# Kernel optimization log

Measured on AMD Instinct MI355X. Metric: run time of the kernel, lower is better.

## Reference

```python
import jax, jax.numpy as jnp
import numpy as np

EPS = 1.1920929e-07  # torch float32 eps used by nn.RMSNorm(elementwise_affine=False)
MAX_LR = 0.01        # default_step_transform_max_lr


def rmsnorm(x):
    return x * jax.lax.rsqrt(jnp.mean(jnp.square(x), axis=-1, keepdims=True) + EPS)


def assoc_scan(gates, inputs):
    # first-order recurrence x_t = gates_t * x_{t-1} + inputs_t along axis=1
    gates = jnp.broadcast_to(gates, inputs.shape)

    def combine(a, b):
        ag, ax = a
        bg, bx = b
        return (ag * bg, bg * ax + bx)

    _, out = jax.lax.associative_scan(combine, (gates, inputs), axis=1)
    return out


def setup_inputs():
    key = jax.random.key(0)
    ks = jax.random.split(key, 12)
    b, t, dim, heads, d, c = 4, 8192, 512, 8, 64, 64
    di = heads * d
    sc_dim = dim ** -0.5
    sc_d = d ** -0.5
    return {
        'seq': jax.random.normal(ks[0], (b, t, dim), jnp.float32),
        'w1': jax.random.normal(ks[1], (d, d), jnp.float32) * sc_d,
        'w2': jax.random.normal(ks[2], (d, d), jnp.float32) * sc_d,
        'Wq': jax.random.normal(ks[3], (dim, di), jnp.float32) * sc_dim,
        'Wkv': jax.random.normal(ks[4], (dim, 2 * di), jnp.float32) * sc_dim,
        'Wstep': jax.random.normal(ks[5], (dim, heads), jnp.float32) * sc_dim,
        'Wmom': jax.random.normal(ks[6], (dim, heads), jnp.float32) * sc_dim,
        'Wdecay': jax.random.normal(ks[7], (dim, heads), jnp.float32) * sc_dim,
        'Wgate': jax.random.normal(ks[8], (dim, heads), jnp.float32) * sc_dim,
        'Wcombine': jax.random.normal(ks[9], (di, dim), jnp.float32) * (di ** -0.5),
        'gamma': jnp.zeros((heads, 1, d), jnp.float32),
        'chunk_size': 64,
    }


def _forward(seq, w1, w2, Wq, Wkv, Wstep, Wmom, Wdecay, Wgate, Wcombine, gamma, c):
    b, t, dim = seq.shape
    heads = Wstep.shape[1]
    d = w1.shape[0]
    n = t // c          # number of chunks (seq_len assumed multiple of chunk_size)
    bh = b * heads

    # ---------------- store_memories ----------------
    s = rmsnorm(seq)  # store_norm
    # adaptive per-token lr: sigmoid * max_lr, per head -> (bh, n, c)
    lr = jax.nn.sigmoid(jnp.einsum('btd,dh->bth', s, Wstep)) * MAX_LR
    lr = lr.transpose(0, 2, 1).reshape(bh, n, c)
    # per-chunk momentum / decay gates from chunk-mean of seq
    s_chunk = s.reshape(b, n, c, dim).mean(axis=2)
    mom_gate = jax.nn.sigmoid(jnp.einsum('bnd,dh->bnh', s_chunk, Wmom)).transpose(0, 2, 1).reshape(bh, n, 1)
    decay = jax.nn.sigmoid(jnp.einsum('bnd,dh->bnh', s_chunk, Wdecay)).transpose(0, 2, 1).reshape(bh, n, 1)
    # keys / values, split heads, chunked -> (bh, n, c, d)
    kv = jnp.einsum('btd,de->bte', s, Wkv)
    k, v = jnp.split(kv, 2, axis=-1)
    split = lambda x: x.reshape(b, t, heads, d).transpose(0, 2, 1, 3).reshape(bh, n, c, d)
    k, v = split(k), split(v)

    def chunk_loss(ws, kc, lrc, vc):
        x = kc @ ws[0]
        x = jax.nn.silu(x) @ ws[1]
        return jnp.sum(jnp.mean(jnp.square(x - vc), axis=-1) * lrc)

    # per-sample (per bh, per chunk) grads of the tiny MLP
    grad_fn = jax.grad(chunk_loss, argnums=0)
    g1, g2 = jax.vmap(jax.vmap(grad_fn, in_axes=(None, 0, 0, 0)), in_axes=(None, 0, 0, 0))((w1, w2), k, lr, v)

    updates = []
    for g in (g1, g2):
        flat = (-g).reshape(bh, n, d * d)        # surprises
        momentum = assoc_scan(mom_gate, flat)     # momentum recurrence
        upd = assoc_scan(1.0 - decay, momentum)   # decayed weight-update recurrence
        updates.append(upd.reshape(bh, n, d, d))

    # ---------------- retrieve_memories ----------------
    r = rmsnorm(seq)[:, c - 1:]                   # retrieve_norm + causal shift
    pad = (-r.shape[1]) % c                       # pad to multiple of chunk_size (= c-1 here)
    r = jnp.pad(r, ((0, 0), (0, pad), (0, 0)))    # (b, n*c, dim)
    q = jnp.einsum('btd,de->bte', r, Wq)
    qs = q.reshape(b, n * c, heads, d).transpose(0, 2, 1, 3).reshape(bh, n, c, d)
    # apply per-chunk fast weights (base + update)
    x = jnp.einsum('bncd,bnde->bnce', qs, w1 + updates[0])
    x = jax.nn.silu(x)
    x = jnp.einsum('bncd,bnde->bnce', x, w2 + updates[1])
    vals = x.reshape(b, heads, n * c, d)
    vals = rmsnorm(vals) * (gamma + 1.0)          # MultiheadRMSNorm (gamma zeros-init)
    gate = jax.nn.sigmoid(jnp.einsum('btd,dh->bth', r, Wgate))  # retrieve_gate
    vals = vals * gate.transpose(0, 2, 1)[..., None]
    out = vals.transpose(0, 2, 1, 3).reshape(b, n * c, heads * d)  # merge heads
    out = jnp.einsum('bte,ed->btd', out, Wcombine)                 # combine_heads
    out = jnp.pad(out, ((0, 0), (c - 1, 0), (0, 0)))[:, :t]       # shift back, crop
    return out


def reference(seq, w1, w2, Wq, Wkv, Wstep, Wmom, Wdecay, Wgate, Wcombine, gamma, chunk_size):
    return _forward(seq, w1, w2, Wq, Wkv, Wstep, Wmom, Wdecay, Wgate, Wcombine, gamma, chunk_size)
```

## Files before the change

### kernel.cpp

```cpp
#include <hip/hip_runtime.h>
#include <cstdint>

#define EPS     1.1920929e-07f
#define MAX_LR  0.01f
#define BB      4
#define TT      8192
#define DIMM    512
#define HH      8
#define DD      64
#define CC      64
#define NN      128
#define BHH     32
#define LDSP    72

typedef __attribute__((ext_vector_type(8))) short short8;
typedef __attribute__((ext_vector_type(4))) float f32x4;

__device__ __forceinline__ float sigmoidf_(float x){ return 1.0f/(1.0f+__expf(-x)); }
__device__ __forceinline__ float bf2f(uint32_t lo16){ return __uint_as_float(lo16<<16); }
__device__ __forceinline__ uint16_t f2bf(float f){
    uint32_t x = __float_as_uint(f);
    return (uint16_t)((x + 0x7fffu + ((x>>16)&1u)) >> 16);
}
__device__ __forceinline__ uint32_t pk2(float a, float b){
    return (uint32_t)f2bf(a) | ((uint32_t)f2bf(b)<<16);
}
__device__ __forceinline__ void gload_lds16(const uint16_t* g, uint16_t* l){
    __builtin_amdgcn_global_load_lds(
        (const __attribute__((address_space(1))) unsigned int*)g,
        (__attribute__((address_space(3))) unsigned int*)l, 16, 0, 0);
}

__device__ __forceinline__ void gemm64(const uint16_t* A, const uint16_t* B,
                                       int strip, int q, int col, f32x4* acc)
{
    #pragma unroll
    for (int ks=0; ks<64; ks+=32){
        short8 af = *(const short8*)&A[(strip*16+col)*LDSP + ks + q*8];
        #pragma unroll
        for (int nt=0;nt<4;nt++){
            short8 bf = *(const short8*)&B[(nt*16+col)*LDSP + ks + q*8];
            acc[nt] = __builtin_amdgcn_mfma_f32_16x16x32_bf16(af, bf, acc[nt], 0,0,0);
        }
    }
}

__device__ __forceinline__ void gemm64g(const uint16_t* __restrict__ Ag,
                                        const uint16_t* B,
                                        int strip, int q, int col, f32x4* acc)
{
    #pragma unroll
    for (int ks=0; ks<64; ks+=32){
        short8 af = *(const short8*)&Ag[(strip*16+col)*DD + ks + q*8];
        #pragma unroll
        for (int nt=0;nt<4;nt++){
            short8 bf = *(const short8*)&B[(nt*16+col)*LDSP + ks + q*8];
            acc[nt] = __builtin_amdgcn_mfma_f32_16x16x32_bf16(af, bf, acc[nt], 0,0,0);
        }
    }
}

__global__ __launch_bounds__(256) void k_scale(
    const float* __restrict__ seq, float* __restrict__ scale,
    uint16_t* __restrict__ sbf)
{
    int wave = threadIdx.x >> 6, lane = threadIdx.x & 63;
    int row = blockIdx.x*4 + wave;
    const float4* sp = (const float4*)&seq[(size_t)row*DIMM + lane*8];
    float4 x0 = sp[0], x1 = sp[1];
    float ss = x0.x*x0.x + x0.y*x0.y + x0.z*x0.z + x0.w*x0.w
             + x1.x*x1.x + x1.y*x1.y + x1.z*x1.z + x1.w*x1.w;
    #pragma unroll
    for (int o=32;o;o>>=1) ss += __shfl_xor(ss,o,64);
    float sc = rsqrtf(ss*(1.0f/DIMM)+EPS);
    if (lane==0) scale[row] = sc;
    uint4 v;
    v.x = pk2(x0.x*sc, x0.y*sc);
    v.y = pk2(x0.z*sc, x0.w*sc);
    v.z = pk2(x1.x*sc, x1.y*sc);
    v.w = pk2(x1.z*sc, x1.w*sc);
    *(uint4*)&sbf[(size_t)row*DIMM + lane*8] = v;
}

__global__ __launch_bounds__(256) void k_pack_wsg(
    const float* __restrict__ Wstep, const float* __restrict__ Wgate,
    uint16_t* __restrict__ wsg)
{
    int g = blockIdx.x*256 + threadIdx.x;
    int j = g >> 9, k = g & 511;
    float v = (j < HH) ? Wstep[k*HH + j] : Wgate[k*HH + (j-HH)];
    wsg[j*DIMM + k] = f2bf(v);
}

__global__ __launch_bounds__(256) void k_pack_w(
    const float* __restrict__ w1, const float* __restrict__ w2,
    uint16_t* __restrict__ w1t_bf, uint16_t* __restrict__ w2t_bf,
    uint16_t* __restrict__ w2b_bf, float* __restrict__ w1t_f,
    float* __restrict__ w2t_f)
{
    __shared__ float t1[64][65];
    __shared__ float t2[64][65];
    int tx = threadIdx.x & 63, ty = threadIdx.x >> 6;
    #pragma unroll
    for (int i=0;i<16;i++){
        int row = ty*16 + i;
        float v1 = w1[row*DD + tx];
        float v2 = w2[row*DD + tx];
        t1[row][tx] = v1;
        t2[row][tx] = v2;
        w2b_bf[row*DD + tx] = f2bf(v2);
    }
    __syncthreads();
    #pragma unroll
    for (int i=0;i<16;i++){
        int row = ty*16 + i;
        float v1 = t1[tx][row];
        float v2 = t2[tx][row];
        w1t_f[row*DD + tx] = v1;
        w1t_bf[row*DD + tx] = f2bf(v1);
        w2t_f[row*DD + tx] = v2;
        w2t_bf[row*DD + tx] = f2bf(v2);
    }
}

__global__ __launch_bounds__(256) void k_lr_gate(
    const uint16_t* __restrict__ sbf, const uint16_t* __restrict__ wsg,
    float* __restrict__ lr_t, float* __restrict__ gate_t)
{
    __shared__ uint16_t Asl[128][LDSP];
    int tid = threadIdx.x;
    int w = tid>>6, lane = tid&63, q = lane>>4, col = lane&15;
    int m0 = blockIdx.x*128;

    f32x4 acc[2];
    acc[0] = (f32x4){0.f,0.f,0.f,0.f};
    acc[1] = (f32x4){0.f,0.f,0.f,0.f};

    for (int k0=0;k0<DIMM;k0+=64){
        #pragma unroll
        for (int s=0;s<4;s++){
            int seg = s*256 + tid;
            int row = seg>>3, kk = seg&7;
            uint4 v = *(const uint4*)&sbf[(size_t)(m0+row)*DIMM + k0 + kk*8];
            *(uint4*)&Asl[row][kk*8] = v;
        }
        __syncthreads();
        #pragma unroll
        for (int ks=0;ks<64;ks+=32){
            short8 bf = *(const short8*)&wsg[(size_t)col*DIMM + k0 + ks + q*8];
            #pragma unroll
            for (int mt=0;mt<2;mt++){
                short8 af = *(const short8*)&Asl[w*32 + mt*16 + col][ks + q*8];
                acc[mt] = __builtin_amdgcn_mfma_f32_16x16x32_bf16(af, bf, acc[mt], 0,0,0);
            }
        }
        __syncthreads();
    }

    #pragma unroll
    for (int mt=0;mt<2;mt++){
        #pragma unroll
        for (int reg=0;reg<4;reg++){
            int m = m0 + w*32 + mt*16 + q*4 + reg;
            int b = m>>13, t = m&8191;
            float val = sigmoidf_(acc[mt][reg]);
            if (col < HH){
                lr_t[(size_t)m*HH + col] = val*MAX_LR;
            } else {
                int j = t-63;
                if (j >= 0)
                    gate_t[((size_t)b*TT + j)*HH + (col-HH)] = val;
            }
        }
    }
}

__global__ __launch_bounds__(512) void k_chunk_gates(
    const float* __restrict__ seq, const float* __restrict__ scale,
    const float* __restrict__ Wmom, const float* __restrict__ Wdecay,
    float* __restrict__ mom, float* __restrict__ dec)
{
    int blk = blockIdx.x;
    int b = blk>>7, n = blk&127;
    int tid = threadIdx.x;
    __shared__ float scl[CC];
    if (tid < CC) scl[tid] = scale[b*TT + n*CC + tid];
    __syncthreads();
    size_t base = ((size_t)b*TT + n*CC)*DIMM + tid;
    float acc=0.f;
    #pragma unroll 8
    for (int j=0;j<CC;j++) acc += seq[base + (size_t)j*DIMM]*scl[j];
    __shared__ float sm[DIMM];
    sm[tid] = acc*(1.0f/CC);
    __syncthreads();
    int wid = tid>>6, lane = tid&63;
    float d1=0.f, d2=0.f;
    #pragma unroll
    for (int i=0;i<8;i++){
        int idx=i*64+lane; float sv=sm[idx];
        d1 += sv*Wmom[idx*HH+wid];
        d2 += sv*Wdecay[idx*HH+wid];
    }
    #pragma unroll
    for (int o=32;o;o>>=1){ d1+=__shfl_down(d1,o,64); d2+=__shfl_down(d2,o,64); }
    if (lane==0){
        mom[(b*HH+wid)*NN + n] = sigmoidf_(d1);
        dec[(b*HH+wid)*NN + n] = sigmoidf_(d2);
    }
}

__global__ __launch_bounds__(256) void k_transpose(
    const float* __restrict__ in, uint16_t* __restrict__ out, int Ncols)
{
    __shared__ float tile[32][33];
    int bx = blockIdx.x*32;
    int by = blockIdx.y*32;
    int lx = threadIdx.x&31, ly = threadIdx.x>>5;
    #pragma unroll
    for (int r=0;r<4;r++)
        tile[ly+8*r][lx] = in[(size_t)(by+ly+8*r)*Ncols + bx+lx];
    __syncthreads();
    #pragma unroll
    for (int r=0;r<4;r++)
        out[(size_t)(bx+ly+8*r)*DIMM + by+lx] = f2bf(tile[lx][ly+8*r]);
}

template<int MODE>
__global__ __launch_bounds__(256) void k_gemm_mfma(
    const void* __restrict__ Av, const uint16_t* __restrict__ Bt,
    const float* __restrict__ scale, void* __restrict__ out0,
    void* __restrict__ out1)
{
    __shared__ uint16_t Asl[128*72];
    __shared__ uint16_t Bsl[128*64];
    __shared__ float sscale[128];
    int tid = threadIdx.x;
    int wave = tid>>6, lane = tid&63;
    int q = lane>>4, col = lane&15;
    int bid = blockIdx.y*gridDim.x + blockIdx.x;
    int xcd = bid & 7, local = bid >> 3;
    int mper = gridDim.y >> 3;
    int m0 = (xcd*mper + local/gridDim.x)*128;
    int n0 = (local%gridDim.x)*128;
    int m_off = (wave&1)*64, n_off = (wave>>1)*64;

    if (MODE==1){
        if (tid<128) sscale[tid] = scale[m0+tid];
        __syncthreads();
    }

    f32x4 acc[4][4];
    #pragma unroll
    for (int i=0;i<4;i++)
        #pragma unroll
        for (int j=0;j<4;j++) acc[i][j] = (f32x4){0.f,0.f,0.f,0.f};

    int srow = wave*32 + (lane>>3);
    int sgs  = lane&7;

    for (int k0=0;k0<DIMM;k0+=64){
        if (MODE!=1){
            const uint16_t* A = (const uint16_t*)Av;
            #pragma unroll
            for (int s=0;s<4;s++){
                int r = srow + s*8;
                gload_lds16(&A[(size_t)(m0+r)*DIMM + k0 + ((sgs ^ (r&7))<<3)],
                            &Asl[(wave*32 + s*8)*64]);
            }
        } else {
            const float* A = (const float*)Av;
            #pragma unroll
            for (int s=0;s<4;s++){
                int seg = s*256 + tid;
                int row = seg>>3, kk = seg&7;
                float sc = sscale[row];
                const float4* ap = (const float4*)&A[(size_t)(m0+row)*DIMM + k0 + kk*8];
                float4 a0 = ap[0], a1 = ap[1];
                uint4 v;
                v.x = pk2(a0.x*sc, a0.y*sc);
                v.y = pk2(a0.z*sc, a0.w*sc);
                v.z = pk2(a1.x*sc, a1.y*sc);
                v.w = pk2(a1.z*sc, a1.w*sc);
                *(uint4*)&Asl[row*72 + kk*8] = v;
            }
        }
        #pragma unroll
        for (int s=0;s<4;s++){
            int r = srow + s*8;
            gload_lds16(&Bt[(size_t)(n0+r)*DIMM + k0 + ((sgs ^ (r&7))<<3)],
                        &Bsl[(wave*32 + s*8)*64]);
        }
        __syncthreads();
        #pragma unroll
        for (int ks=0;ks<64;ks+=32){
            short8 af[4], bf[4];
            int g = q + (ks>>3);
            #pragma unroll
            for (int mt=0;mt<4;mt++){
                int r = m_off + mt*16 + col;
                if (MODE==1)
                    af[mt] = *(const short8*)&Asl[r*72 + ks + q*8];
                else
                    af[mt] = *(const short8*)&Asl[r*64 + ((g ^ (r&7))<<3)];
            }
            #pragma unroll
            for (int nt=0;nt<4;nt++){
                int rb = n_off + nt*16 + col;
                bf[nt] = *(const short8*)&Bsl[rb*64 + ((g ^ (rb&7))<<3)];
            }
            #pragma unroll
            for (int mt=0;mt<4;mt++)
                #pragma unroll
                for (int nt=0;nt<4;nt++)
                    acc[mt][nt] = __builtin_amdgcn_mfma_f32_16x16x32_bf16(
                        af[mt], bf[nt], acc[mt][nt], 0, 0, 0);
        }
        __syncthreads();
    }

    #pragma unroll
    for (int mt=0;mt<4;mt++){
        #pragma unroll
        for (int reg=0;reg<4;reg++){
            int m = m0 + m_off + mt*16 + q*4 + reg;
            int b = m>>13, t = m&8191;
            if (MODE==0){
                #pragma unroll
                for (int nt=0;nt<4;nt++){
                    int e = n0 + n_off + nt*16 + col;
                    uint16_t* basep = (uint16_t*)((e<512) ? out0 : out1);
                    int ee = e & 511;
                    int h = ee>>6, dk = ee&63;
                    basep[((size_t)(b*HH+h)*TT + t)*DD + dk] = f2bf(acc[mt][nt][reg]);
                }
            } else if (MODE==1){
                int j = t-63;
                if (j>=0){
                    #pragma unroll
                    for (int nt=0;nt<4;nt++){
                        int e = n0 + n_off + nt*16 + col;
                        int h = e>>6, dk = e&63;
                        ((uint16_t*)out0)[((size_t)(b*HH+h)*TT + j)*DD + dk] = f2bf(acc[mt][nt][reg]);
                    }
                }
            } else {
                int tp = t + 63;
                if (tp < TT){
                    #pragma unroll
                    for (int nt=0;nt<4;nt++){
                        int e = n0 + n_off + nt*16 + col;
                        ((float*)out0)[((size_t)b*TT + tp)*DIMM + e] = acc[mt][nt][reg];
                    }
                }
            }
        }
    }
}

__global__ __launch_bounds__(256) void k_grad(
    const uint16_t* __restrict__ kbuf, const uint16_t* __restrict__ vbuf,
    const float* __restrict__ lr_t, const uint16_t* __restrict__ w1t_bf,
    const uint16_t* __restrict__ w2t_bf, const uint16_t* __restrict__ w2b_bf,
    uint16_t* __restrict__ g1T, uint16_t* __restrict__ g2T)
{
    __shared__ uint16_t lds[5*64*LDSP];
    __shared__ float lr_sh[64];
    uint16_t* kcB  = lds + 0*64*LDSP;
    uint16_t* kcT  = lds + 1*64*LDSP;
    uint16_t* vB   = lds + 2*64*LDSP;
    uint16_t* hA   = lds + 3*64*LDSP;
    uint16_t* hB   = lds + 4*64*LDSP;
    uint16_t* dxA  = kcB;
    uint16_t* dxB  = vB;
    uint16_t* dx1T = hB;

    int bhn = blockIdx.x;
    int bh = bhn>>7, n = bhn&127;
    int b = bh>>3, h = bh&7;
    int tid = threadIdx.x, tx = tid&15, ty = tid>>4;
    int w = tid>>6, lane = tid&63, q = lane>>4, col = lane&15;
    size_t cbase = ((size_t)bh*TT + n*CC)*DD;

    #pragma unroll
    for (int r=0;r<4;r++){
        int row = ty*4+r;
        ushort4 k4 = *(const ushort4*)&kbuf[cbase + row*DD + tx*4];
        *(ushort4*)&kcB[row*LDSP + tx*4] = k4;
        kcT[(tx*4+0)*LDSP + row] = k4.x;
        kcT[(tx*4+1)*LDSP + row] = k4.y;
        kcT[(tx*4+2)*LDSP + row] = k4.z;
        kcT[(tx*4+3)*LDSP + row] = k4.w;
        ushort4 v4 = *(const ushort4*)&vbuf[cbase + row*DD + tx*4];
        *(ushort4*)&vB[row*LDSP + tx*4] = v4;
    }
    if (tid < 64) lr_sh[tid] = lr_t[((size_t)b*TT + n*CC + tid)*HH + h];
    __syncthreads();

    f32x4 a1[4];
    #pragma unroll
    for (int i=0;i<4;i++) a1[i]=(f32x4){0.f,0.f,0.f,0.f};
    gemm64g(w1t_bf, kcB, w, q, col, a1);
    float sg[16], hr[16];
    #pragma unroll
    for (int nt=0;nt<4;nt++)
        #pragma unroll
        for (int reg=0;reg<4;reg++){
            int idx = nt*4+reg;
            float x = a1[nt][reg];
            float sgm = sigmoidf_(x);
            sg[idx]=sgm; hr[idx]=x*sgm;
            int d1 = w*16 + q*4 + reg;
            int token = nt*16 + col;
            uint16_t hv = f2bf(x*sgm);
            hA[d1*LDSP + token] = hv;
            hB[token*LDSP + d1] = hv;
        }
    __syncthreads();

    f32x4 a2[4];
    #pragma unroll
    for (int i=0;i<4;i++) a2[i]=(f32x4){0.f,0.f,0.f,0.f};
    gemm64g(w2t_bf, hB, w, q, col, a2);
    __syncthreads();
    #pragma unroll
    for (int nt=0;nt<4;nt++)
        #pragma unroll
        for (int reg=0;reg<4;reg++){
            int d2 = w*16 + q*4 + reg;
            int token = nt*16 + col;
            float vv = bf2f(vB[token*LDSP + d2]);
            float dx = (2.0f/DD)*lr_sh[token]*(a2[nt][reg]-vv);
            uint16_t dv = f2bf(dx);
            dxA[d2*LDSP + token] = dv;
            dxB[token*LDSP + d2] = dv;
        }
    __syncthreads();

    f32x4 a3[4];
    #pragma unroll
    for (int i=0;i<4;i++) a3[i]=(f32x4){0.f,0.f,0.f,0.f};
    gemm64(dxA, hA, w, q, col, a3);
    f32x4 a4[4];
    #pragma unroll
    for (int i=0;i<4;i++) a4[i]=(f32x4){0.f,0.f,0.f,0.f};
    gemm64g(w2b_bf, dxB, w, q, col, a4);

    size_t gb = (size_t)bhn*4096;
    #pragma unroll
    for (int nt=0;nt<4;nt++)
        #pragma unroll
        for (int reg=0;reg<4;reg++){
            int d2 = w*16 + q*4 + reg;
            int d1 = nt*16 + col;
            g2T[gb + d2*DD + d1] = f2bf(-a3[nt][reg]);
        }
    #pragma unroll
    for (int nt=0;nt<4;nt++)
        #pragma unroll
        for (int reg=0;reg<4;reg++){
            int idx = nt*4+reg;
            int d1 = w*16 + q*4 + reg;
            int token = nt*16 + col;
            float dsl = sg[idx] + hr[idx]*(1.f-sg[idx]);
            dx1T[d1*LDSP + token] = f2bf(a4[nt][reg]*dsl);
        }
    __syncthreads();

    f32x4 a5[4];
    #pragma unroll
    for (int i=0;i<4;i++) a5[i]=(f32x4){0.f,0.f,0.f,0.f};
    gemm64(dx1T, kcT, w, q, col, a5);
    #pragma unroll
    for (int nt=0;nt<4;nt++)
        #pragma unroll
        for (int reg=0;reg<4;reg++){
            int d1 = w*16 + q*4 + reg;
            int p  = nt*16 + col;
            g1T[gb + d1*DD + p] = f2bf(-a5[nt][reg]);
        }
}

__global__ __launch_bounds__(256) void k_scan(
    uint16_t* __restrict__ g1, uint16_t* __restrict__ g2,
    const float* __restrict__ mom, const float* __restrict__ dec)
{
    int blk = blockIdx.x;
    int arr = blk>>7; int rem = blk&127;
    int bh = rem>>2; int eg = rem&3;
    int e4 = eg*1024 + threadIdx.x*4;
    uint16_t* gp = arr ? g2 : g1;
    __shared__ float smg[NN], sdc[NN];
    if (threadIdx.x < NN){
        smg[threadIdx.x] = mom[bh*NN+threadIdx.x];
        sdc[threadIdx.x] = 1.f - dec[bh*NN+threadIdx.x];
    }
    __syncthreads();
    size_t base = (size_t)bh*NN*4096 + e4;
    float m0=0.f,m1=0.f,m2=0.f,m3=0.f, u0=0.f,u1=0.f,u2=0.f,u3=0.f;
    uint2 p0 = *(const uint2*)&gp[base];
    uint2 p1 = *(const uint2*)&gp[base + 4096];
    uint2 p2 = *(const uint2*)&gp[base + 2*4096];
    uint2 p3 = *(const uint2*)&gp[base + 3*4096];
    for (int t=0; t<NN; t+=4){
        uint2 c0=p0, c1=p1, c2=p2, c3=p3;
        if (t+4 < NN){
            p0 = *(const uint2*)&gp[base + (size_t)(t+4)*4096];
            p1 = *(const uint2*)&gp[base + (size_t)(t+5)*4096];
            p2 = *(const uint2*)&gp[base + (size_t)(t+6)*4096];
            p3 = *(const uint2*)&gp[base + (size_t)(t+7)*4096];
        }
        #pragma unroll
        for (int j=0;j<4;j++){
            uint2 c = (j==0)?c0:(j==1)?c1:(j==2)?c2:c3;
            float g = smg[t+j], d = sdc[t+j];
            float v0 = bf2f(c.x&0xffffu), v1 = bf2f(c.x>>16);
            float v2 = bf2f(c.y&0xffffu), v3 = bf2f(c.y>>16);
            m0 = fmaf(g,m0,v0); u0 = fmaf(d,u0,m0);
            m1 = fmaf(g,m1,v1); u1 = fmaf(d,u1,m1);
            m2 = fmaf(g,m2,v2); u2 = fmaf(d,u2,m2);
            m3 = fmaf(g,m3,v3); u3 = fmaf(d,u3,m3);
            uint2 r; r.x = pk2(u0,u1); r.y = pk2(u2,u3);
            *(uint2*)&gp[base + (size_t)(t+j)*4096] = r;
        }
    }
}

__global__ __launch_bounds__(256) void k_retrieve(
    const uint16_t* __restrict__ qbuf, const uint16_t* __restrict__ u1T,
    const uint16_t* __restrict__ u2T, const float* __restrict__ w1Tf,
    const float* __restrict__ w2Tf, const float* __restrict__ gamma,
    const float* __restrict__ gate_t, uint16_t* __restrict__ y)
{
    __shared__ uint16_t qc[64*LDSP];
    __shared__ uint16_t W1s[64*LDSP];
    __shared__ uint16_t W2s[64*LDSP];
    __shared__ uint16_t hB[64*LDSP];
    __shared__ float gate_sh[64], gam_sh[64];
    int bhn = blockIdx.x;
    int bh = bhn>>7, n = bhn&127;
    int b = bh>>3, h = bh&7;
    int tid = threadIdx.x, tx = tid&15, ty = tid>>4;
    int w = tid>>6, lane = tid&63, q = lane>>4, col = lane&15;
    size_t cbase = ((size_t)bh*TT + n*CC)*DD;
    size_t ub = (size_t)bhn*4096;

    #pragma unroll
    for (int r=0;r<4;r++){
        int row = ty*4+r;
        *(ushort4*)&qc[row*LDSP + tx*4] =
            *(const ushort4*)&qbuf[cbase + row*DD + tx*4];
        ushort4 u14 = *(const ushort4*)&u1T[ub + row*DD + tx*4];
        float4 w1v = *(const float4*)&w1Tf[row*DD + tx*4];
        ushort4 s1;
        s1.x = f2bf(w1v.x + bf2f(u14.x));
        s1.y = f2bf(w1v.y + bf2f(u14.y));
        s1.z = f2bf(w1v.z + bf2f(u14.z));
        s1.w = f2bf(w1v.w + bf2f(u14.w));
        *(ushort4*)&W1s[row*LDSP + tx*4] = s1;
        ushort4 u24 = *(const ushort4*)&u2T[ub + row*DD + tx*4];
        float4 w2v = *(const float4*)&w2Tf[row*DD + tx*4];
        ushort4 s2;
        s2.x = f2bf(w2v.x + bf2f(u24.x));
        s2.y = f2bf(w2v.y + bf2f(u24.y));
        s2.z = f2bf(w2v.z + bf2f(u24.z));
        s2.w = f2bf(w2v.w + bf2f(u24.w));
        *(ushort4*)&W2s[row*LDSP + tx*4] = s2;
    }
    if (tid < 64){
        gate_sh[tid] = gate_t[((size_t)b*TT + n*CC + tid)*HH + h];
        gam_sh[tid]  = gamma[h*DD + tid];
    }
    __syncthreads();

    f32x4 a1[4];
    #pragma unroll
    for (int i=0;i<4;i++) a1[i]=(f32x4){0.f,0.f,0.f,0.f};
    gemm64(qc, W1s, w, q, col, a1);
    #pragma unroll
    for (int nt=0;nt<4;nt++)
        #pragma unroll
        for (int reg=0;reg<4;reg++){
            float x = a1[nt][reg];
            int token = w*16 + q*4 + reg;
            int d1 = nt*16 + col;
            hB[token*LDSP + d1] = f2bf(x*sigmoidf_(x));
        }
    __syncthreads();

    f32x4 a2[4];
    #pragma unroll
    for (int i=0;i<4;i++) a2[i]=(f32x4){0.f,0.f,0.f,0.f};
    gemm64(hB, W2s, w, q, col, a2);
    #pragma unroll
    for (int reg=0;reg<4;reg++){
        float p = 0.f;
        #pragma unroll
        for (int nt=0;nt<4;nt++) p += a2[nt][reg]*a2[nt][reg];
        p += __shfl_xor(p,1,64);
        p += __shfl_xor(p,2,64);
        p += __shfl_xor(p,4,64);
        p += __shfl_xor(p,8,64);
        float sclv = rsqrtf(p*(1.0f/DD)+EPS);
        int token = w*16 + q*4 + reg;
        float gt = gate_sh[token];
        size_t yb = ((size_t)b*TT + n*CC + token)*DIMM + h*DD;
        #pragma unroll
        for (int nt=0;nt<4;nt++){
            int d2 = nt*16 + col;
            y[yb + d2] = f2bf(a2[nt][reg]*sclv*(1.f+gam_sh[d2])*gt);
        }
    }
}

__global__ __launch_bounds__(256) void k_zero(
    uint16_t* __restrict__ qbuf, float* __restrict__ out, float* __restrict__ gate_t)
{
    int g = blockIdx.x*256 + threadIdx.x;
    const int QN = BHH*63*DD;
    const int ON = BB*63*DIMM;
    const int GN = BB*63*HH;
    if (g < QN){
        int bh = g/4032; int r = g - bh*4032;
        int j = 8129 + (r>>6); int dk = r&63;
        qbuf[((size_t)bh*TT + j)*DD + dk] = 0;
    } else if (g < QN+ON){
        int g2i = g - QN;
        int b = g2i/(63*512); int r = g2i - b*63*512;
        int t = r>>9; int e = r&511;
        out[((size_t)b*TT + t)*DIMM + e] = 0.f;
    } else if (g < QN+ON+GN){
        int g3 = g - QN - ON;
        int b = g3/(63*HH); int r = g3 - b*63*HH;
        int j = 8129 + (r>>3); int hh = r&7;
        gate_t[((size_t)b*TT + j)*HH + hh] = 0.f;
    }
}

extern "C" void kernel_launch(void* const* d_in, const int* in_sizes, int n_in,
                              void* d_out, int out_size, void* d_ws, size_t ws_size,
                              hipStream_t stream)
{
    (void)in_sizes; (void)n_in; (void)out_size; (void)ws_size;
    const float* seq    = (const float*)d_in[0];
    const float* w1     = (const float*)d_in[1];
    const float* w2     = (const float*)d_in[2];
    const float* Wq     = (const float*)d_in[3];
    const float* Wkv    = (const float*)d_in[4];
    const float* Wstep  = (const float*)d_in[5];
    const float* Wmom   = (const float*)d_in[6];
    const float* Wdecay = (const float*)d_in[7];
    const float* Wgate  = (const float*)d_in[8];
    const float* Wcomb  = (const float*)d_in[9];
    const float* gamma  = (const float*)d_in[10];
    float* out = (float*)d_out;

    float* scale = (float*)d_ws;
    float* lr_t  = scale + 32768;
    float* gate_t= lr_t + 262144;
    float* mom   = gate_t + 262144;
    float* dec   = mom + 4096;
    uint16_t* btkv = (uint16_t*)(dec + 4096);
    uint16_t* btq  = btkv + 1024*512;
    uint16_t* btc  = btq  + 512*512;
    uint16_t* kb = btc + 512*512;
    uint16_t* vb = kb + 16777216;
    uint16_t* g1 = vb + 16777216;
    uint16_t* g2 = g1 + 16777216;
    uint16_t* sbf = g1;
    uint16_t* wsg = g2;
    uint16_t* w1t_bf = btkv;
    uint16_t* w2t_bf = btkv + 4096;
    uint16_t* w2b_bf = btkv + 8192;
    float*    w1t_f  = (float*)(btkv + 16384);
    float*    w2t_f  = w1t_f + 4096;

    k_transpose<<<dim3(32,16), 256, 0, stream>>>(Wkv,   btkv, 1024);
    k_transpose<<<dim3(16,16), 256, 0, stream>>>(Wq,    btq,  512);
    k_transpose<<<dim3(16,16), 256, 0, stream>>>(Wcomb, btc,  512);
    k_pack_wsg  <<<32, 256, 0, stream>>>(Wstep, Wgate, wsg);
    k_scale     <<<8192, 256, 0, stream>>>(seq, scale, sbf);
    k_lr_gate   <<<256, 256, 0, stream>>>(sbf, wsg, lr_t, gate_t);
    k_chunk_gates<<<BB*NN, 512, 0, stream>>>(seq, scale, Wmom, Wdecay, mom, dec);
    k_gemm_mfma<0><<<dim3(8, 256), 256, 0, stream>>>(sbf, btkv, nullptr, kb, vb);
    k_pack_w <<<1, 256, 0, stream>>>(w1, w2, w1t_bf, w2t_bf, w2b_bf, w1t_f, w2t_f);
    k_grad   <<<BHH*NN, 256, 0, stream>>>(kb, vb, lr_t, w1t_bf, w2t_bf, w2b_bf, g1, g2);
    k_scan   <<<256, 256, 0, stream>>>(g1, g2, mom, dec);
    k_gemm_mfma<1><<<dim3(4, 256), 256, 0, stream>>>(seq, btq, scale, kb , nullptr);
    k_zero   <<<1017, 256, 0, stream>>>(kb , out, gate_t);
    k_retrieve<<<BHH*NN, 256, 0, stream>>>(kb , g1, g2, w1t_f, w2t_f, gamma, gate_t, vb );
    k_gemm_mfma<2><<<dim3(4, 256), 256, 0, stream>>>(vb , btc, nullptr, out, nullptr);
}
```

Measured before the change: 371.7 us.

## Merge weight-prep kernels, stage KV GEMM epilogue through LDS, use bf16 chunk means

Five small weight packing/transpose launches are folded into one k_prep kernel to cut launch overhead, and the fp32 weight copies move to their own workspace region so they no longer alias btkv. The mode-0 GEMM epilogue writes the tile to LDS and then does 16-byte coalesced stores to k/v, replacing scattered 2-byte stores. k_chunk_gates now reads the bf16 normalized sequence instead of fp32 seq times scale, halving its read traffic at a small precision cost.

```diff
diff --git a/kernel.cpp b/kernel.cpp
--- a/kernel.cpp
+++ b/kernel.cpp
@@ -60,6 +60,66 @@
     }
 }
 
+__global__ __launch_bounds__(256) void k_prep(
+    const float* __restrict__ Wkv, const float* __restrict__ Wq,
+    const float* __restrict__ Wcomb, const float* __restrict__ Wstep,
+    const float* __restrict__ Wgate, const float* __restrict__ w1,
+    const float* __restrict__ w2,
+    uint16_t* __restrict__ btkv, uint16_t* __restrict__ btq,
+    uint16_t* __restrict__ btc, uint16_t* __restrict__ wsg,
+    uint16_t* __restrict__ w1t_bf, uint16_t* __restrict__ w2t_bf,
+    uint16_t* __restrict__ w2b_bf, float* __restrict__ w1t_f,
+    float* __restrict__ w2t_f)
+{
+    __shared__ float tile[32][33];
+    __shared__ float t1[64][65];
+    __shared__ float t2[64][65];
+    int blk = blockIdx.x;
+    if (blk < 1024){
+        const float* in; uint16_t* out; int Ncols; int i;
+        if (blk < 512){ in=Wkv; out=btkv; Ncols=1024; i=blk; }
+        else if (blk < 768){ in=Wq; out=btq; Ncols=512; i=blk-512; }
+        else { in=Wcomb; out=btc; Ncols=512; i=blk-768; }
+        int nx = Ncols>>5;
+        int bx = (i % nx)*32, by = (i / nx)*32;
+        int lx = threadIdx.x&31, ly = threadIdx.x>>5;
+        #pragma unroll
+        for (int r=0;r<4;r++)
+            tile[ly+8*r][lx] = in[(size_t)(by+ly+8*r)*Ncols + bx+lx];
+        __syncthreads();
+        #pragma unroll
+        for (int r=0;r<4;r++)
+            out[(size_t)(bx+ly+8*r)*DIMM + by+lx] = f2bf(tile[lx][ly+8*r]);
+    } else if (blk < 1056){
+        int g = (blk-1024)*256 + threadIdx.x;
+        int j = g >> 9, k = g & 511;
+        float v = (j < HH) ? Wstep[k*HH + j] : Wgate[k*HH + (j-HH)];
+        wsg[j*DIMM + k] = f2bf(v);
+    } else {
+        int tx = threadIdx.x & 63, ty = threadIdx.x >> 6;
+        #pragma unroll
+        for (int i=0;i<16;i++){
+            int row = ty*16 + i;
+            float v1 = w1[row*DD + tx];
+            float v2 = w2[row*DD + tx];
+            t1[row][tx] = v1;
+            t2[row][tx] = v2;
+            w2b_bf[row*DD + tx] = f2bf(v2);
+        }
+        __syncthreads();
+        #pragma unroll
+        for (int i=0;i<16;i++){
+            int row = ty*16 + i;
+            float v1 = t1[tx][row];
+            float v2 = t2[tx][row];
+            w1t_f[row*DD + tx] = v1;
+            w1t_bf[row*DD + tx] = f2bf(v1);
+            w2t_f[row*DD + tx] = v2;
+            w2t_bf[row*DD + tx] = f2bf(v2);
+        }
+    }
+}
+
 __global__ __launch_bounds__(256) void k_scale(
     const float* __restrict__ seq, float* __restrict__ scale,
     uint16_t* __restrict__ sbf)
@@ -80,47 +140,6 @@
     v.z = pk2(x1.x*sc, x1.y*sc);
     v.w = pk2(x1.z*sc, x1.w*sc);
     *(uint4*)&sbf[(size_t)row*DIMM + lane*8] = v;
-}
-
-__global__ __launch_bounds__(256) void k_pack_wsg(
-    const float* __restrict__ Wstep, const float* __restrict__ Wgate,
-    uint16_t* __restrict__ wsg)
-{
-    int g = blockIdx.x*256 + threadIdx.x;
-    int j = g >> 9, k = g & 511;
-    float v = (j < HH) ? Wstep[k*HH + j] : Wgate[k*HH + (j-HH)];
-    wsg[j*DIMM + k] = f2bf(v);
-}
-
-__global__ __launch_bounds__(256) void k_pack_w(
-    const float* __restrict__ w1, const float* __restrict__ w2,
-    uint16_t* __restrict__ w1t_bf, uint16_t* __restrict__ w2t_bf,
-    uint16_t* __restrict__ w2b_bf, float* __restrict__ w1t_f,
-    float* __restrict__ w2t_f)
-{
-    __shared__ float t1[64][65];
-    __shared__ float t2[64][65];
-    int tx = threadIdx.x & 63, ty = threadIdx.x >> 6;
-    #pragma unroll
-    for (int i=0;i<16;i++){
-        int row = ty*16 + i;
-        float v1 = w1[row*DD + tx];
-        float v2 = w2[row*DD + tx];
-        t1[row][tx] = v1;
-        t2[row][tx] = v2;
-        w2b_bf[row*DD + tx] = f2bf(v2);
-    }
-    __syncthreads();
-    #pragma unroll
-    for (int i=0;i<16;i++){
-        int row = ty*16 + i;
-        float v1 = t1[tx][row];
-        float v2 = t2[tx][row];
-        w1t_f[row*DD + tx] = v1;
-        w1t_bf[row*DD + tx] = f2bf(v1);
-        w2t_f[row*DD + tx] = v2;
-        w2t_bf[row*DD + tx] = f2bf(v2);
-    }
 }
 
 __global__ __launch_bounds__(256) void k_lr_gate(
@@ -176,20 +195,17 @@
 }
 
 __global__ __launch_bounds__(512) void k_chunk_gates(
-    const float* __restrict__ seq, const float* __restrict__ scale,
+    const uint16_t* __restrict__ sbf,
     const float* __restrict__ Wmom, const float* __restrict__ Wdecay,
     float* __restrict__ mom, float* __restrict__ dec)
 {
     int blk = blockIdx.x;
     int b = blk>>7, n = blk&127;
     int tid = threadIdx.x;
-    __shared__ float scl[CC];
-    if (tid < CC) scl[tid] = scale[b*TT + n*CC + tid];
-    __syncthreads();
     size_t base = ((size_t)b*TT + n*CC)*DIMM + tid;
     float acc=0.f;
     #pragma unroll 8
-    for (int j=0;j<CC;j++) acc += seq[base + (size_t)j*DIMM]*scl[j];
+    for (int j=0;j<CC;j++) acc += bf2f(sbf[base + (size_t)j*DIMM]);
     __shared__ float sm[DIMM];
     sm[tid] = acc*(1.0f/CC);
     __syncthreads();
@@ -207,22 +223,6 @@
         mom[(b*HH+wid)*NN + n] = sigmoidf_(d1);
         dec[(b*HH+wid)*NN + n] = sigmoidf_(d2);
     }
-}
-
-__global__ __launch_bounds__(256) void k_transpose(
-    const float* __restrict__ in, uint16_t* __restrict__ out, int Ncols)
-{
-    __shared__ float tile[32][33];
-    int bx = blockIdx.x*32;
-    int by = blockIdx.y*32;
-    int lx = threadIdx.x&31, ly = threadIdx.x>>5;
-    #pragma unroll
-    for (int r=0;r<4;r++)
-        tile[ly+8*r][lx] = in[(size_t)(by+ly+8*r)*Ncols + bx+lx];
-    __syncthreads();
-    #pragma unroll
-    for (int r=0;r<4;r++)
-        out[(size_t)(bx+ly+8*r)*DIMM + by+lx] = f2bf(tile[lx][ly+8*r]);
 }
 
 template<int MODE>
@@ -231,8 +231,9 @@
     const float* __restrict__ scale, void* __restrict__ out0,
     void* __restrict__ out1)
 {
-    __shared__ uint16_t Asl[128*72];
-    __shared__ uint16_t Bsl[128*64];
+    __shared__ __align__(16) uint16_t shmem[128*72 + 128*64];
+    uint16_t* Asl = shmem;
+    uint16_t* Bsl = shmem + 128*72;
     __shared__ float sscale[128];
     int tid = threadIdx.x;
     int wave = tid>>6, lane = tid&63;
@@ -318,38 +319,57 @@
         __syncthreads();
     }
 
-    #pragma unroll
-    for (int mt=0;mt<4;mt++){
-        #pragma unroll
-        for (int reg=0;reg<4;reg++){
-            int m = m0 + m_off + mt*16 + q*4 + reg;
-            int b = m>>13, t = m&8191;
-            if (MODE==0){
+    if (MODE==0){
+        #pragma unroll
+        for (int mt=0;mt<4;mt++)
+            #pragma unroll
+            for (int reg=0;reg<4;reg++){
+                int lrow = m_off + mt*16 + q*4 + reg;
                 #pragma unroll
                 for (int nt=0;nt<4;nt++){
-                    int e = n0 + n_off + nt*16 + col;
-                    uint16_t* basep = (uint16_t*)((e<512) ? out0 : out1);
-                    int ee = e & 511;
-                    int h = ee>>6, dk = ee&63;
-                    basep[((size_t)(b*HH+h)*TT + t)*DD + dk] = f2bf(acc[mt][nt][reg]);
+                    int le = n_off + nt*16 + col;
+                    shmem[lrow*128 + le] = f2bf(acc[mt][nt][reg]);
                 }
-            } else if (MODE==1){
-                int j = t-63;
-                if (j>=0){
-                    #pragma unroll
-                    for (int nt=0;nt<4;nt++){
-                        int e = n0 + n_off + nt*16 + col;
-                        int h = e>>6, dk = e&63;
-                        ((uint16_t*)out0)[((size_t)(b*HH+h)*TT + j)*DD + dk] = f2bf(acc[mt][nt][reg]);
+            }
+        __syncthreads();
+        uint16_t* basep = (uint16_t*)((n0 < 512) ? out0 : out1);
+        int h0 = (n0 & 511) >> 6;
+        #pragma unroll
+        for (int p=0;p<8;p++){
+            int idx = p*256 + tid;
+            int lrow = idx >> 4, seg = idx & 15;
+            int m = m0 + lrow;
+            int b = m>>13, t = m&8191;
+            int h = h0 + (seg>>3);
+            int dk = (seg&7)*8;
+            uint4 v = *(const uint4*)&shmem[lrow*128 + seg*8];
+            *(uint4*)&basep[((size_t)(b*HH+h)*TT + t)*DD + dk] = v;
+        }
+    } else {
+        #pragma unroll
+        for (int mt=0;mt<4;mt++){
+            #pragma unroll
+            for (int reg=0;reg<4;reg++){
+                int m = m0 + m_off + mt*16 + q*4 + reg;
+                int b = m>>13, t = m&8191;
+                if (MODE==1){
+                    int j = t-63;
+                    if (j>=0){
+                        #pragma unroll
+                        for (int nt=0;nt<4;nt++){
+                            int e = n0 + n_off + nt*16 + col;
+                            int h = e>>6, dk = e&63;
+                            ((uint16_t*)out0)[((size_t)(b*HH+h)*TT + j)*DD + dk] = f2bf(acc[mt][nt][reg]);
+                        }
                     }
-                }
-            } else {
-                int tp = t + 63;
-                if (tp < TT){
-                    #pragma unroll
-                    for (int nt=0;nt<4;nt++){
-                        int e = n0 + n_off + nt*16 + col;
-                        ((float*)out0)[((size_t)b*TT + tp)*DIMM + e] = acc[mt][nt][reg];
+                } else {
+                    int tp = t + 63;
+                    if (tp < TT){
+                        #pragma unroll
+                        for (int nt=0;nt<4;nt++){
+                            int e = n0 + n_off + nt*16 + col;
+                            ((float*)out0)[((size_t)b*TT + tp)*DIMM + e] = acc[mt][nt][reg];
+                        }
                     }
                 }
             }
@@ -659,7 +679,12 @@
     float* gate_t= lr_t + 262144;
     float* mom   = gate_t + 262144;
     float* dec   = mom + 4096;
-    uint16_t* btkv = (uint16_t*)(dec + 4096);
+    float* w1t_f = dec + 4096;
+    float* w2t_f = w1t_f + 4096;
+    uint16_t* w1t_bf = (uint16_t*)(w2t_f + 4096);
+    uint16_t* w2t_bf = w1t_bf + 4096;
+    uint16_t* w2b_bf = w2t_bf + 4096;
+    uint16_t* btkv = w2b_bf + 4096;
     uint16_t* btq  = btkv + 1024*512;
     uint16_t* btc  = btq  + 512*512;
     uint16_t* kb = btc + 512*512;
@@ -668,21 +693,14 @@
     uint16_t* g2 = g1 + 16777216;
     uint16_t* sbf = g1;
     uint16_t* wsg = g2;
-    uint16_t* w1t_bf = btkv;
-    uint16_t* w2t_bf = btkv + 4096;
-    uint16_t* w2b_bf = btkv + 8192;
-    float*    w1t_f  = (float*)(btkv + 16384);
-    float*    w2t_f  = w1t_f + 4096;
-
-    k_transpose<<<dim3(32,16), 256, 0, stream>>>(Wkv,   btkv, 1024);
-    k_transpose<<<dim3(16,16), 256, 0, stream>>>(Wq,    btq,  512);
-    k_transpose<<<dim3(16,16), 256, 0, stream>>>(Wcomb, btc,  512);
-    k_pack_wsg  <<<32, 256, 0, stream>>>(Wstep, Wgate, wsg);
+
+    k_prep <<<1057, 256, 0, stream>>>(Wkv, Wq, Wcomb, Wstep, Wgate, w1, w2,
+                                      btkv, btq, btc, wsg,
+                                      w1t_bf, w2t_bf, w2b_bf, w1t_f, w2t_f);
     k_scale     <<<8192, 256, 0, stream>>>(seq, scale, sbf);
     k_lr_gate   <<<256, 256, 0, stream>>>(sbf, wsg, lr_t, gate_t);
-    k_chunk_gates<<<BB*NN, 512, 0, stream>>>(seq, scale, Wmom, Wdecay, mom, dec);
+    k_chunk_gates<<<BB*NN, 512, 0, stream>>>(sbf, Wmom, Wdecay, mom, dec);
     k_gemm_mfma<0><<<dim3(8, 256), 256, 0, stream>>>(sbf, btkv, nullptr, kb, vb);
-    k_pack_w <<<1, 256, 0, stream>>>(w1, w2, w1t_bf, w2t_bf, w2b_bf, w1t_f, w2t_f);
     k_grad   <<<BHH*NN, 256, 0, stream>>>(kb, vb, lr_t, w1t_bf, w2t_bf, w2b_bf, g1, g2);
     k_scan   <<<256, 256, 0, stream>>>(g1, g2, mom, dec);
     k_gemm_mfma<1><<<dim3(4, 256), 256, 0, stream>>>(seq, btq, scale, kb , nullptr);
```

After: 357.7 us. -3.8%, faster.
